# Optimization experiments

Measured on AMD Instinct MI355X. Metric: run time of the kernel, lower is better.

## Reference

```python
import jax, jax.numpy as jnp
import numpy as np

NUM_HEADS = 16
ROPE_BASE = 10000.0

def rotate_half(x):
    h = x.shape[-1] // 2
    return jnp.concatenate([-x[..., h:], x[..., :h]], axis=-1)

def rope_cos_sin(seq_len, head_dim, dtype):
    inv_freq = 1.0 / (ROPE_BASE ** (jnp.arange(0, head_dim, 2, dtype=jnp.float32) / head_dim))
    t = jnp.arange(seq_len, dtype=jnp.float32)
    freqs = jnp.outer(t, inv_freq)              # [N, hd/2]
    emb = jnp.concatenate([freqs, freqs], -1)   # [N, hd]
    return jnp.cos(emb).astype(dtype), jnp.sin(emb).astype(dtype)

def setup_inputs() -> dict:
    key = jax.random.key(0)
    ks = jax.random.split(key, 5)
    B, N, D = 2, 2048, 1024
    s = 1.0 / np.sqrt(D)
    return {
        "x": jax.random.normal(ks[0], (B, N, D), jnp.float32),
        "attention_mask": jnp.ones((B, N), jnp.int32),
        "Wq": jax.random.normal(ks[1], (D, D), jnp.float32) * s,
        "Wk": jax.random.normal(ks[2], (D, D), jnp.float32) * s,
        "Wv": jax.random.normal(ks[3], (D, D), jnp.float32) * s,
        "Wo": jax.random.normal(ks[4], (D, D), jnp.float32) * s,
    }

def reference(x, attention_mask, Wq, Wk, Wv, Wo):
    B, N, D = x.shape
    H = NUM_HEADS
    hd = D // H
    scale = hd ** -0.5
    # projections (nn.Linear: x @ W.T), split heads -> [B, H, N, hd]
    q = jnp.einsum('bnd,ed->bne', x, Wq).reshape(B, N, H, hd).transpose(0, 2, 1, 3)
    k = jnp.einsum('bnd,ed->bne', x, Wk).reshape(B, N, H, hd).transpose(0, 2, 1, 3)
    v = jnp.einsum('bnd,ed->bne', x, Wv).reshape(B, N, H, hd).transpose(0, 2, 1, 3)
    cos, sin = rope_cos_sin(N, hd, x.dtype)     # [N, hd]
    cos = cos[None, None]; sin = sin[None, None]
    q = q * cos + rotate_half(q) * sin
    k = k * cos + rotate_half(k) * sin
    attn = jnp.einsum('bhqd,bhkd->bhqk', q, k) * scale
    mask = attention_mask.astype(bool)[:, None, None, :]        # [B,1,1,N]
    attn = jnp.where(mask, attn, -jnp.inf)
    all_masked = (attention_mask.sum(-1) == 0)[:, None, None, None]
    attn = jnp.where(all_masked, 0.0, attn)
    attn = jax.nn.softmax(attn, axis=-1)
    out = jnp.einsum('bhqk,bhkd->bhqd', attn, v)
    out = out.transpose(0, 2, 1, 3).reshape(B, N, D)
    return jnp.einsum('bnd,ed->bne', out, Wo)
```

## Files before the change

### kernel.cpp

```cpp
#include <hip/hip_runtime.h>
#include <math.h>

#define BATCH 2
#define SEQ   2048
#define DM    1024
#define NH    16
#define HD    64
#define MTOT  (BATCH*SEQ)

typedef short v8s __attribute__((ext_vector_type(8)));
typedef short v4s __attribute__((ext_vector_type(4)));
typedef float v4f __attribute__((ext_vector_type(4)));

#define MFMA16(a, b, c) __builtin_amdgcn_mfma_f32_16x16x32_bf16((a), (b), (c), 0, 0, 0)

__device__ __forceinline__ short f2b(float f) {
    union { float f; unsigned u; } v; v.f = f;
    return (short)((v.u + 0x8000u) >> 16);
}

__global__ __launch_bounds__(256) void cvt_all_kernel(
    const float* __restrict__ x,  const float* __restrict__ wq,
    const float* __restrict__ wk, const float* __restrict__ wv,
    const float* __restrict__ wo, short* __restrict__ dst)
{
    int i = blockIdx.x * 256 + threadIdx.x;
    const float* src; int off;
    if (i < (1 << 19)) { src = x; off = i; }
    else {
        int j = i - (1 << 19);
        int wsel = j >> 17;
        off = j & ((1 << 17) - 1);
        src = (wsel == 0) ? wq : (wsel == 1) ? wk : (wsel == 2) ? wv : wo;
    }
    const float4* s4 = (const float4*)src;
    float4 a = s4[2 * off], b = s4[2 * off + 1];
    v8s p;
    p[0] = f2b(a.x); p[1] = f2b(a.y); p[2] = f2b(a.z); p[3] = f2b(a.w);
    p[4] = f2b(b.x); p[5] = f2b(b.y); p[6] = f2b(b.z); p[7] = f2b(b.w);
    *(v8s*)&dst[8 * i] = p;
}

__global__ __launch_bounds__(256, 2) void kv_rope_mfma(
    const short* __restrict__ xb, const short* __restrict__ Wkb,
    const short* __restrict__ Wvb, short* __restrict__ K, short* __restrict__ Vt)
{
    const int zz = blockIdx.z;
    const short* __restrict__ Wb = zz ? Wvb : Wkb;
    const int m0 = blockIdx.x * 128, e00 = blockIdx.y * 128;
    const int tid = threadIdx.x;
    const int w = tid >> 6, lane = tid & 63, lq = lane >> 4, lr = lane & 15;
    const int wm = w >> 1, wn = w & 1;

    __shared__ union {
        struct { short As[128][32]; short Bs[128][32]; } p1;
        short Css[128][136];
    } u;

    v4f acc[4][4];
    #pragma unroll
    for (int i = 0; i < 4; ++i)
        for (int j = 0; j < 4; ++j)
            for (int r = 0; r < 4; ++r) acc[i][j][r] = 0.f;

    const int arow = tid >> 1, aseg = (tid & 1) * 16;
    for (int k0 = 0; k0 < DM; k0 += 32) {
        v8s a0 = *(const v8s*)&xb[(size_t)(m0 + arow) * DM + k0 + aseg];
        v8s a1 = *(const v8s*)&xb[(size_t)(m0 + arow) * DM + k0 + aseg + 8];
        v8s b0 = *(const v8s*)&Wb[(size_t)(e00 + arow) * DM + k0 + aseg];
        v8s b1 = *(const v8s*)&Wb[(size_t)(e00 + arow) * DM + k0 + aseg + 8];
        __syncthreads();
        *(v8s*)&u.p1.As[arow][aseg] = a0;
        *(v8s*)&u.p1.As[arow][aseg + 8] = a1;
        *(v8s*)&u.p1.Bs[arow][aseg] = b0;
        *(v8s*)&u.p1.Bs[arow][aseg + 8] = b1;
        __syncthreads();
        v8s af[4], bf[4];
        #pragma unroll
        for (int i = 0; i < 4; ++i)
            af[i] = *(const v8s*)&u.p1.As[64 * wm + 16 * i + lr][8 * lq];
        #pragma unroll
        for (int j = 0; j < 4; ++j)
            bf[j] = *(const v8s*)&u.p1.Bs[64 * wn + 16 * j + lr][8 * lq];
        #pragma unroll
        for (int i = 0; i < 4; ++i)
            #pragma unroll
            for (int j = 0; j < 4; ++j)
                acc[i][j] = MFMA16(af[i], bf[j], acc[i][j]);
    }
    __syncthreads();

    const int b = m0 >> 11, n00 = m0 & (SEQ - 1);
    const float LN1E4_D32 = 0.28782313662425572f;

    if (zz == 0) {
        float f0 = expf(-(float)lr * LN1E4_D32);
        float f1 = expf(-(float)(16 + lr) * LN1E4_D32);
        #pragma unroll
        for (int i = 0; i < 4; ++i) {
            #pragma unroll
            for (int r = 0; r < 4; ++r) {
                int row = 64 * wm + 16 * i + 4 * lq + r;
                int n = n00 + row;
                float c0v, s0v, c1v, s1v;
                sincosf((float)n * f0, &s0v, &c0v);
                sincosf((float)n * f1, &s1v, &c1v);
                float q0 = acc[i][0][r], q1 = acc[i][1][r];
                float q2 = acc[i][2][r], q3 = acc[i][3][r];
                u.Css[row][64 * wn + lr]      = f2b(q0 * c0v - q2 * s0v);
                u.Css[row][64 * wn + 16 + lr] = f2b(q1 * c1v - q3 * s1v);
                u.Css[row][64 * wn + 32 + lr] = f2b(q2 * c0v + q0 * s0v);
                u.Css[row][64 * wn + 48 + lr] = f2b(q3 * c1v + q1 * s1v);
            }
        }
        __syncthreads();
        int row = tid >> 1, hh = tid & 1;
        int h = (e00 >> 6) + hh;
        int n = n00 + row;
        size_t base = (((size_t)(b * NH + h)) * SEQ + n) * HD;
        #pragma unroll
        for (int p = 0; p < 8; ++p)
            *(v8s*)&K[base + 8 * p] = *(const v8s*)&u.Css[row][64 * hh + 8 * p];
    } else {
        #pragma unroll
        for (int i = 0; i < 4; ++i) {
            #pragma unroll
            for (int j = 0; j < 4; ++j) {
                v4s t;
                #pragma unroll
                for (int r = 0; r < 4; ++r) t[r] = f2b(acc[i][j][r]);
                *(v4s*)&u.Css[64 * wn + 16 * j + lr][64 * wm + 16 * i + 4 * lq] = t;
            }
        }
        __syncthreads();
        int c = tid >> 1, half = (tid & 1) * 64;
        int h = (e00 + c) >> 6, d = (e00 + c) & 63;
        size_t base = (((size_t)(b * NH + h)) * HD + d) * SEQ + n00 + half;
        #pragma unroll
        for (int p = 0; p < 8; ++p)
            *(v8s*)&Vt[base + 8 * p] = *(const v8s*)&u.Css[c][half + 8 * p];
    }
}

__global__ __launch_bounds__(256, 2) void attn_mfma(
    const short* __restrict__ xb, const short* __restrict__ Wqb,
    const short* __restrict__ K, const short* __restrict__ Vt,
    const int* __restrict__ mask, short* __restrict__ O)
{
    const int m0 = blockIdx.x * 128, h = blockIdx.y, e0 = h * 64;
    const int b = m0 >> 11, n0 = m0 & (SEQ - 1), bh = b * NH + h;
    const int tid = threadIdx.x;
    const int w = tid >> 6, lane = tid & 63, lq = lane >> 4, lr = lane & 15;
    const int sr = tid >> 2, sc = (tid & 3) * 8;

    __shared__ union {
        struct { short As[128][32]; short Bs[64][32]; } p1;
        struct { short Ks[64][72]; short Vs[64][72]; } p2;
    } u;
    __shared__ short Ps[128][72];
    __shared__ float mbias[64];

    v4f acc[2][4];
    #pragma unroll
    for (int s = 0; s < 2; ++s)
        for (int nt = 0; nt < 4; ++nt)
            for (int r = 0; r < 4; ++r) acc[s][nt][r] = 0.f;

    for (int k0 = 0; k0 < DM; k0 += 32) {
        v8s a0 = *(const v8s*)&xb[(size_t)(m0 + sr) * DM + k0 + sc];
        v8s a1 = *(const v8s*)&xb[(size_t)(m0 + 64 + sr) * DM + k0 + sc];
        v8s bv = *(const v8s*)&Wqb[(size_t)(e0 + sr) * DM + k0 + sc];
        __syncthreads();
        *(v8s*)&u.p1.As[sr][sc] = a0;
        *(v8s*)&u.p1.As[64 + sr][sc] = a1;
        *(v8s*)&u.p1.Bs[sr][sc] = bv;
        __syncthreads();
        v8s aw0 = *(const v8s*)&u.p1.As[16 * w + lr][lq * 8];
        v8s aw1 = *(const v8s*)&u.p1.As[64 + 16 * w + lr][lq * 8];
        #pragma unroll
        for (int nt = 0; nt < 4; ++nt) {
            v8s bb = *(const v8s*)&u.p1.Bs[16 * nt + lr][lq * 8];
            acc[0][nt] = MFMA16(aw0, bb, acc[0][nt]);
            acc[1][nt] = MFMA16(aw1, bb, acc[1][nt]);
        }
    }

    {
        const float LN1E4_D32 = 0.28782313662425572f;
        const float QSCALE = 0.18033688011112042f;
        float f0 = expf(-(float)lr * LN1E4_D32);
        float f1 = expf(-(float)(16 + lr) * LN1E4_D32);
        #pragma unroll
        for (int s = 0; s < 2; ++s) {
            #pragma unroll
            for (int r = 0; r < 4; ++r) {
                int n = n0 + 64 * s + 16 * w + 4 * lq + r;
                float c0v, s0v, c1v, s1v;
                sincosf((float)n * f0, &s0v, &c0v);
                sincosf((float)n * f1, &s1v, &c1v);
                float q0 = acc[s][0][r], q1 = acc[s][1][r];
                float q2 = acc[s][2][r], q3 = acc[s][3][r];
                Ps[64 * s + 16 * w + 4 * lq + r][lr]      = f2b(QSCALE * (q0 * c0v - q2 * s0v));
                Ps[64 * s + 16 * w + 4 * lq + r][16 + lr] = f2b(QSCALE * (q1 * c1v - q3 * s1v));
                Ps[64 * s + 16 * w + 4 * lq + r][32 + lr] = f2b(QSCALE * (q2 * c0v + q0 * s0v));
                Ps[64 * s + 16 * w + 4 * lq + r][48 + lr] = f2b(QSCALE * (q3 * c1v + q1 * s1v));
            }
        }
    }
    v8s aq[2][2];
    #pragma unroll
    for (int s = 0; s < 2; ++s)
        #pragma unroll
        for (int ks = 0; ks < 2; ++ks)
            aq[s][ks] = *(const v8s*)&Ps[64 * s + 16 * w + lr][32 * ks + 8 * lq];

    float lacc[2][4];
    #pragma unroll
    for (int s = 0; s < 2; ++s)
        for (int r = 0; r < 4; ++r) lacc[s][r] = 0.f;
    v4f o[2][4];
    #pragma unroll
    for (int s = 0; s < 2; ++s)
        for (int nt = 0; nt < 4; ++nt)
            for (int r = 0; r < 4; ++r) o[s][nt][r] = 0.f;

    const int r2 = tid >> 2, cc = (tid & 3) * 16;
    const int pr = 16 * (r2 & 3) + (r2 >> 2);
    const short* __restrict__ Kb = K + (size_t)bh * SEQ * HD;
    const short* __restrict__ Vb = Vt + (size_t)bh * HD * SEQ;

    v8s k1 = *(const v8s*)&Kb[(size_t)r2 * HD + cc];
    v8s k2 = *(const v8s*)&Kb[(size_t)r2 * HD + cc + 8];
    v8s v1 = *(const v8s*)&Vb[(size_t)r2 * SEQ + cc];
    v8s v2 = *(const v8s*)&Vb[(size_t)r2 * SEQ + cc + 8];
    int mnext = (tid < 64) ? mask[b * SEQ + tid] : 0;

    for (int c0 = 0; c0 < SEQ; c0 += 64) {
        __syncthreads();
        *(v8s*)&u.p2.Ks[pr][cc] = k1;
        *(v8s*)&u.p2.Ks[pr][cc + 8] = k2;
        *(v8s*)&u.p2.Vs[r2][cc] = v1;
        *(v8s*)&u.p2.Vs[r2][cc + 8] = v2;
        if (tid < 64) mbias[tid] = mnext ? -24.0f : -1e30f;
        __syncthreads();
        if (c0 + 64 < SEQ) {
            k1 = *(const v8s*)&Kb[(size_t)(c0 + 64 + r2) * HD + cc];
            k2 = *(const v8s*)&Kb[(size_t)(c0 + 64 + r2) * HD + cc + 8];
            v1 = *(const v8s*)&Vb[(size_t)r2 * SEQ + c0 + 64 + cc];
            v2 = *(const v8s*)&Vb[(size_t)r2 * SEQ + c0 + 64 + cc + 8];
            if (tid < 64) mnext = mask[b * SEQ + c0 + 64 + tid];
        }

        v8s kf[2][4], vf[2][4];
        #pragma unroll
        for (int ks = 0; ks < 2; ++ks)
            #pragma unroll
            for (int nt = 0; nt < 4; ++nt) {
                kf[ks][nt] = *(const v8s*)&u.p2.Ks[16 * nt + lr][32 * ks + 8 * lq];
                vf[ks][nt] = *(const v8s*)&u.p2.Vs[16 * nt + lr][32 * ks + 8 * lq];
            }
        float bias[4];
        #pragma unroll
        for (int nt = 0; nt < 4; ++nt) bias[nt] = mbias[4 * lr + nt];

        #pragma unroll
        for (int s = 0; s < 2; ++s) {
            v4f sv[4];
            #pragma unroll
            for (int nt = 0; nt < 4; ++nt)
                for (int r = 0; r < 4; ++r) sv[nt][r] = 0.f;
            #pragma unroll
            for (int ks = 0; ks < 2; ++ks)
                #pragma unroll
                for (int nt = 0; nt < 4; ++nt)
                    sv[nt] = MFMA16(aq[s][ks], kf[ks][nt], sv[nt]);

            #pragma unroll
            for (int r = 0; r < 4; ++r) {
                v4s pk;
                #pragma unroll
                for (int nt = 0; nt < 4; ++nt) {
                    float p = exp2f(sv[nt][r] + bias[nt]);
                    lacc[s][r] += p;
                    pk[nt] = f2b(p);
                }
                *(v4s*)&Ps[64 * s + 16 * w + 4 * lq + r][4 * lr] = pk;
            }
            #pragma unroll
            for (int ks = 0; ks < 2; ++ks) {
                v8s a = *(const v8s*)&Ps[64 * s + 16 * w + lr][32 * ks + 8 * lq];
                #pragma unroll
                for (int nt = 0; nt < 4; ++nt)
                    o[s][nt] = MFMA16(a, vf[ks][nt], o[s][nt]);
            }
        }
    }

    #pragma unroll
    for (int s = 0; s < 2; ++s) {
        #pragma unroll
        for (int r = 0; r < 4; ++r) {
            float l = lacc[s][r];
            l += __shfl_xor(l, 1);
            l += __shfl_xor(l, 2);
            l += __shfl_xor(l, 4);
            l += __shfl_xor(l, 8);
            float inv = (l > 0.f) ? 1.f / l : 0.f;
            int qrow = 64 * s + 16 * w + 4 * lq + r;
            #pragma unroll
            for (int nt = 0; nt < 4; ++nt)
                O[(size_t)(m0 + qrow) * DM + h * HD + 16 * nt + lr] =
                    f2b(o[s][nt][r] * inv);
        }
    }
}

__global__ __launch_bounds__(256, 2) void oproj_mfma(
    const short* __restrict__ O, const short* __restrict__ Wob,
    float* __restrict__ out)
{
    const int m0 = blockIdx.x * 64, e00 = blockIdx.y * 128;
    const int tid = threadIdx.x;
    const int w = tid >> 6, lane = tid & 63, lq = lane >> 4, lr = lane & 15;

    __shared__ short As[64][32];
    __shared__ short Bs[128][32];

    v4f acc[4][2];
    #pragma unroll
    for (int i = 0; i < 4; ++i)
        for (int j = 0; j < 2; ++j)
            for (int r = 0; r < 4; ++r) acc[i][j][r] = 0.f;

    const int arow = tid >> 2, aseg = (tid & 3) * 8;
    const int brow = tid >> 1, bseg = (tid & 1) * 16;
    for (int k0 = 0; k0 < DM; k0 += 32) {
        v8s a0 = *(const v8s*)&O[(size_t)(m0 + arow) * DM + k0 + aseg];
        v8s b0 = *(const v8s*)&Wob[(size_t)(e00 + brow) * DM + k0 + bseg];
        v8s b1 = *(const v8s*)&Wob[(size_t)(e00 + brow) * DM + k0 + bseg + 8];
        __syncthreads();
        *(v8s*)&As[arow][aseg] = a0;
        *(v8s*)&Bs[brow][bseg] = b0;
        *(v8s*)&Bs[brow][bseg + 8] = b1;
        __syncthreads();
        v8s af[4], bf[2];
        #pragma unroll
        for (int i = 0; i < 4; ++i)
            af[i] = *(const v8s*)&As[16 * i + lr][8 * lq];
        #pragma unroll
        for (int j = 0; j < 2; ++j)
            bf[j] = *(const v8s*)&Bs[32 * w + 16 * j + lr][8 * lq];
        #pragma unroll
        for (int i = 0; i < 4; ++i)
            #pragma unroll
            for (int j = 0; j < 2; ++j)
                acc[i][j] = MFMA16(af[i], bf[j], acc[i][j]);
    }

    #pragma unroll
    for (int i = 0; i < 4; ++i)
        #pragma unroll
        for (int r = 0; r < 4; ++r) {
            int m = m0 + 16 * i + 4 * lq + r;
            #pragma unroll
            for (int j = 0; j < 2; ++j)
                out[(size_t)m * DM + e00 + 32 * w + 16 * j + lr] = acc[i][j][r];
        }
}

extern "C" void kernel_launch(void* const* d_in, const int* in_sizes, int n_in,
                              void* d_out, int out_size, void* d_ws, size_t ws_size,
                              hipStream_t stream)
{
    const float* x    = (const float*)d_in[0];
    const int*   mask = (const int*)d_in[1];
    const float* Wq   = (const float*)d_in[2];
    const float* Wk   = (const float*)d_in[3];
    const float* Wv   = (const float*)d_in[4];
    const float* Wo   = (const float*)d_in[5];
    float* out = (float*)d_out;

    short* xb  = (short*)d_ws;
    short* Wqb = xb  + (size_t)MTOT * DM;
    short* Wkb = Wqb + (size_t)DM * DM;
    short* Wvb = Wkb + (size_t)DM * DM;
    short* Wob = Wvb + (size_t)DM * DM;
    short* O   = Wob + (size_t)DM * DM;
    short* K  = (short*)d_out;
    short* Vt = K + (size_t)MTOT * DM;

    cvt_all_kernel<<<4096, 256, 0, stream>>>(x, Wq, Wk, Wv, Wo, xb);

    dim3 g1(MTOT / 128, DM / 128, 2);
    kv_rope_mfma<<<g1, 256, 0, stream>>>(xb, Wkb, Wvb, K, Vt);

    dim3 g2(MTOT / 128, NH);
    attn_mfma<<<g2, 256, 0, stream>>>(xb, Wqb, K, Vt, mask, O);

    dim3 g3(MTOT / 64, DM / 128);
    oproj_mfma<<<g3, 256, 0, stream>>>(O, Wob, out);
}
```

Measured before the change: 221.8 us.

## Split attention block across 8 waves and use fast range-reduced RoPE sincos

The attention kernel now launches 512 threads per 128-query block, so each wave owns 16 query rows instead of 32. This halves per-wave accumulator registers and spreads K/V tile loads across more threads, aiming for higher occupancy and latency hiding. RoPE sin/cos is computed by reducing the angle to revolutions with floor and calling __sinf/__cosf instead of full-precision sincosf, in both the KV and Q paths. The trade-offs are some loss of accuracy at large angles and the Wq tile being loaded by only half the threads.

```diff
diff --git a/kernel.cpp b/kernel.cpp
--- a/kernel.cpp
+++ b/kernel.cpp
@@ -18,6 +18,17 @@
     union { float f; unsigned u; } v; v.f = f;
     return (short)((v.u + 0x8000u) >> 16);
 }
+
+__device__ __forceinline__ void rope_cs(int n, float f_rev, float* c, float* s) {
+    float rev = (float)n * f_rev;
+    float t = rev - floorf(rev);
+    float ang = t * 6.283185307179586f;
+    *c = __cosf(ang);
+    *s = __sinf(ang);
+}
+
+#define L2_1E4_D32 0.4152410118609203f
+#define INV2PI     0.15915494309189535f
 
 __global__ __launch_bounds__(256) void cvt_all_kernel(
     const float* __restrict__ x,  const float* __restrict__ wq,
@@ -91,11 +102,10 @@
     __syncthreads();
 
     const int b = m0 >> 11, n00 = m0 & (SEQ - 1);
-    const float LN1E4_D32 = 0.28782313662425572f;
 
     if (zz == 0) {
-        float f0 = expf(-(float)lr * LN1E4_D32);
-        float f1 = expf(-(float)(16 + lr) * LN1E4_D32);
+        float f0 = exp2f(-(float)lr * L2_1E4_D32) * INV2PI;
+        float f1 = exp2f(-(float)(16 + lr) * L2_1E4_D32) * INV2PI;
         #pragma unroll
         for (int i = 0; i < 4; ++i) {
             #pragma unroll
@@ -103,8 +113,8 @@
                 int row = 64 * wm + 16 * i + 4 * lq + r;
                 int n = n00 + row;
                 float c0v, s0v, c1v, s1v;
-                sincosf((float)n * f0, &s0v, &c0v);
-                sincosf((float)n * f1, &s1v, &c1v);
+                rope_cs(n, f0, &c0v, &s0v);
+                rope_cs(n, f1, &c1v, &s1v);
                 float q0 = acc[i][0][r], q1 = acc[i][1][r];
                 float q2 = acc[i][2][r], q3 = acc[i][3][r];
                 u.Css[row][64 * wn + lr]      = f2b(q0 * c0v - q2 * s0v);
@@ -142,7 +152,7 @@
     }
 }
 
-__global__ __launch_bounds__(256, 2) void attn_mfma(
+__global__ __launch_bounds__(512, 4) void attn_mfma(
     const short* __restrict__ xb, const short* __restrict__ Wqb,
     const short* __restrict__ K, const short* __restrict__ Vt,
     const int* __restrict__ mask, short* __restrict__ O)
@@ -151,7 +161,6 @@
     const int b = m0 >> 11, n0 = m0 & (SEQ - 1), bh = b * NH + h;
     const int tid = threadIdx.x;
     const int w = tid >> 6, lane = tid & 63, lq = lane >> 4, lr = lane & 15;
-    const int sr = tid >> 2, sc = (tid & 3) * 8;
 
     __shared__ union {
         struct { short As[128][32]; short Bs[64][32]; } p1;
@@ -160,94 +169,79 @@
     __shared__ short Ps[128][72];
     __shared__ float mbias[64];
 
-    v4f acc[2][4];
-    #pragma unroll
-    for (int s = 0; s < 2; ++s)
-        for (int nt = 0; nt < 4; ++nt)
-            for (int r = 0; r < 4; ++r) acc[s][nt][r] = 0.f;
-
+    v4f acc[4];
+    #pragma unroll
+    for (int nt = 0; nt < 4; ++nt)
+        for (int r = 0; r < 4; ++r) acc[nt][r] = 0.f;
+
+    const int sr = tid >> 2, sc = (tid & 3) * 8;
+    const int br = (tid - 256) >> 2, bc = (tid & 3) * 8;
     for (int k0 = 0; k0 < DM; k0 += 32) {
         v8s a0 = *(const v8s*)&xb[(size_t)(m0 + sr) * DM + k0 + sc];
-        v8s a1 = *(const v8s*)&xb[(size_t)(m0 + 64 + sr) * DM + k0 + sc];
-        v8s bv = *(const v8s*)&Wqb[(size_t)(e0 + sr) * DM + k0 + sc];
+        v8s bv;
+        if (tid >= 256)
+            bv = *(const v8s*)&Wqb[(size_t)(e0 + br) * DM + k0 + bc];
         __syncthreads();
         *(v8s*)&u.p1.As[sr][sc] = a0;
-        *(v8s*)&u.p1.As[64 + sr][sc] = a1;
-        *(v8s*)&u.p1.Bs[sr][sc] = bv;
-        __syncthreads();
-        v8s aw0 = *(const v8s*)&u.p1.As[16 * w + lr][lq * 8];
-        v8s aw1 = *(const v8s*)&u.p1.As[64 + 16 * w + lr][lq * 8];
+        if (tid >= 256)
+            *(v8s*)&u.p1.Bs[br][bc] = bv;
+        __syncthreads();
+        v8s aw = *(const v8s*)&u.p1.As[16 * w + lr][8 * lq];
         #pragma unroll
         for (int nt = 0; nt < 4; ++nt) {
-            v8s bb = *(const v8s*)&u.p1.Bs[16 * nt + lr][lq * 8];
-            acc[0][nt] = MFMA16(aw0, bb, acc[0][nt]);
-            acc[1][nt] = MFMA16(aw1, bb, acc[1][nt]);
+            v8s bb = *(const v8s*)&u.p1.Bs[16 * nt + lr][8 * lq];
+            acc[nt] = MFMA16(aw, bb, acc[nt]);
         }
     }
 
     {
-        const float LN1E4_D32 = 0.28782313662425572f;
         const float QSCALE = 0.18033688011112042f;
-        float f0 = expf(-(float)lr * LN1E4_D32);
-        float f1 = expf(-(float)(16 + lr) * LN1E4_D32);
-        #pragma unroll
-        for (int s = 0; s < 2; ++s) {
-            #pragma unroll
-            for (int r = 0; r < 4; ++r) {
-                int n = n0 + 64 * s + 16 * w + 4 * lq + r;
-                float c0v, s0v, c1v, s1v;
-                sincosf((float)n * f0, &s0v, &c0v);
-                sincosf((float)n * f1, &s1v, &c1v);
-                float q0 = acc[s][0][r], q1 = acc[s][1][r];
-                float q2 = acc[s][2][r], q3 = acc[s][3][r];
-                Ps[64 * s + 16 * w + 4 * lq + r][lr]      = f2b(QSCALE * (q0 * c0v - q2 * s0v));
-                Ps[64 * s + 16 * w + 4 * lq + r][16 + lr] = f2b(QSCALE * (q1 * c1v - q3 * s1v));
-                Ps[64 * s + 16 * w + 4 * lq + r][32 + lr] = f2b(QSCALE * (q2 * c0v + q0 * s0v));
-                Ps[64 * s + 16 * w + 4 * lq + r][48 + lr] = f2b(QSCALE * (q3 * c1v + q1 * s1v));
-            }
-        }
-    }
-    v8s aq[2][2];
-    #pragma unroll
-    for (int s = 0; s < 2; ++s)
-        #pragma unroll
-        for (int ks = 0; ks < 2; ++ks)
-            aq[s][ks] = *(const v8s*)&Ps[64 * s + 16 * w + lr][32 * ks + 8 * lq];
-
-    float lacc[2][4];
-    #pragma unroll
-    for (int s = 0; s < 2; ++s)
-        for (int r = 0; r < 4; ++r) lacc[s][r] = 0.f;
-    v4f o[2][4];
-    #pragma unroll
-    for (int s = 0; s < 2; ++s)
-        for (int nt = 0; nt < 4; ++nt)
-            for (int r = 0; r < 4; ++r) o[s][nt][r] = 0.f;
-
-    const int r2 = tid >> 2, cc = (tid & 3) * 16;
-    const int pr = 16 * (r2 & 3) + (r2 >> 2);
+        float f0 = exp2f(-(float)lr * L2_1E4_D32) * INV2PI;
+        float f1 = exp2f(-(float)(16 + lr) * L2_1E4_D32) * INV2PI;
+        #pragma unroll
+        for (int r = 0; r < 4; ++r) {
+            int row = 16 * w + 4 * lq + r;
+            int n = n0 + row;
+            float c0v, s0v, c1v, s1v;
+            rope_cs(n, f0, &c0v, &s0v);
+            rope_cs(n, f1, &c1v, &s1v);
+            float q0 = acc[0][r], q1 = acc[1][r];
+            float q2 = acc[2][r], q3 = acc[3][r];
+            Ps[row][lr]      = f2b(QSCALE * (q0 * c0v - q2 * s0v));
+            Ps[row][16 + lr] = f2b(QSCALE * (q1 * c1v - q3 * s1v));
+            Ps[row][32 + lr] = f2b(QSCALE * (q2 * c0v + q0 * s0v));
+            Ps[row][48 + lr] = f2b(QSCALE * (q3 * c1v + q1 * s1v));
+        }
+    }
+    v8s aq[2];
+    #pragma unroll
+    for (int ks = 0; ks < 2; ++ks)
+        aq[ks] = *(const v8s*)&Ps[16 * w + lr][32 * ks + 8 * lq];
+
+    float lacc[4] = {0.f, 0.f, 0.f, 0.f};
+    v4f o[4];
+    #pragma unroll
+    for (int nt = 0; nt < 4; ++nt)
+        for (int r = 0; r < 4; ++r) o[nt][r] = 0.f;
+
+    const int kr = tid >> 3, kc = (tid & 7) * 8;
+    const int pr = 16 * (kr & 3) + (kr >> 2);
     const short* __restrict__ Kb = K + (size_t)bh * SEQ * HD;
     const short* __restrict__ Vb = Vt + (size_t)bh * HD * SEQ;
 
-    v8s k1 = *(const v8s*)&Kb[(size_t)r2 * HD + cc];
-    v8s k2 = *(const v8s*)&Kb[(size_t)r2 * HD + cc + 8];
-    v8s v1 = *(const v8s*)&Vb[(size_t)r2 * SEQ + cc];
-    v8s v2 = *(const v8s*)&Vb[(size_t)r2 * SEQ + cc + 8];
+    v8s k1 = *(const v8s*)&Kb[(size_t)kr * HD + kc];
+    v8s v1 = *(const v8s*)&Vb[(size_t)kr * SEQ + kc];
     int mnext = (tid < 64) ? mask[b * SEQ + tid] : 0;
 
     for (int c0 = 0; c0 < SEQ; c0 += 64) {
         __syncthreads();
-        *(v8s*)&u.p2.Ks[pr][cc] = k1;
-        *(v8s*)&u.p2.Ks[pr][cc + 8] = k2;
-        *(v8s*)&u.p2.Vs[r2][cc] = v1;
-        *(v8s*)&u.p2.Vs[r2][cc + 8] = v2;
+        *(v8s*)&u.p2.Ks[pr][kc] = k1;
+        *(v8s*)&u.p2.Vs[kr][kc] = v1;
         if (tid < 64) mbias[tid] = mnext ? -24.0f : -1e30f;
         __syncthreads();
         if (c0 + 64 < SEQ) {
-            k1 = *(const v8s*)&Kb[(size_t)(c0 + 64 + r2) * HD + cc];
-            k2 = *(const v8s*)&Kb[(size_t)(c0 + 64 + r2) * HD + cc + 8];
-            v1 = *(const v8s*)&Vb[(size_t)r2 * SEQ + c0 + 64 + cc];
-            v2 = *(const v8s*)&Vb[(size_t)r2 * SEQ + c0 + 64 + cc + 8];
+            k1 = *(const v8s*)&Kb[(size_t)(c0 + 64 + kr) * HD + kc];
+            v1 = *(const v8s*)&Vb[(size_t)kr * SEQ + c0 + 64 + kc];
             if (tid < 64) mnext = mask[b * SEQ + c0 + 64 + tid];
         }
 
@@ -263,55 +257,49 @@
         #pragma unroll
         for (int nt = 0; nt < 4; ++nt) bias[nt] = mbias[4 * lr + nt];
 
-        #pragma unroll
-        for (int s = 0; s < 2; ++s) {
-            v4f sv[4];
+        v4f sv[4];
+        #pragma unroll
+        for (int nt = 0; nt < 4; ++nt)
+            for (int r = 0; r < 4; ++r) sv[nt][r] = 0.f;
+        #pragma unroll
+        for (int ks = 0; ks < 2; ++ks)
             #pragma unroll
             for (int nt = 0; nt < 4; ++nt)
-                for (int r = 0; r < 4; ++r) sv[nt][r] = 0.f;
-            #pragma unroll
-            for (int ks = 0; ks < 2; ++ks)
-                #pragma unroll
-                for (int nt = 0; nt < 4; ++nt)
-                    sv[nt] = MFMA16(aq[s][ks], kf[ks][nt], sv[nt]);
-
-            #pragma unroll
-            for (int r = 0; r < 4; ++r) {
-                v4s pk;
-                #pragma unroll
-                for (int nt = 0; nt < 4; ++nt) {
-                    float p = exp2f(sv[nt][r] + bias[nt]);
-                    lacc[s][r] += p;
-                    pk[nt] = f2b(p);
-                }
-                *(v4s*)&Ps[64 * s + 16 * w + 4 * lq + r][4 * lr] = pk;
+                sv[nt] = MFMA16(aq[ks], kf[ks][nt], sv[nt]);
+
+        #pragma unroll
+        for (int r = 0; r < 4; ++r) {
+            v4s pk;
+            #pragma unroll
+            for (int nt = 0; nt < 4; ++nt) {
+                float p = exp2f(sv[nt][r] + bias[nt]);
+                lacc[r] += p;
+                pk[nt] = f2b(p);
             }
-            #pragma unroll
-            for (int ks = 0; ks < 2; ++ks) {
-                v8s a = *(const v8s*)&Ps[64 * s + 16 * w + lr][32 * ks + 8 * lq];
-                #pragma unroll
-                for (int nt = 0; nt < 4; ++nt)
-                    o[s][nt] = MFMA16(a, vf[ks][nt], o[s][nt]);
-            }
-        }
-    }
-
-    #pragma unroll
-    for (int s = 0; s < 2; ++s) {
-        #pragma unroll
-        for (int r = 0; r < 4; ++r) {
-            float l = lacc[s][r];
-            l += __shfl_xor(l, 1);
-            l += __shfl_xor(l, 2);
-            l += __shfl_xor(l, 4);
-            l += __shfl_xor(l, 8);
-            float inv = (l > 0.f) ? 1.f / l : 0.f;
-            int qrow = 64 * s + 16 * w + 4 * lq + r;
+            *(v4s*)&Ps[16 * w + 4 * lq + r][4 * lr] = pk;
+        }
+        #pragma unroll
+        for (int ks = 0; ks < 2; ++ks) {
+            v8s a = *(const v8s*)&Ps[16 * w + lr][32 * ks + 8 * lq];
             #pragma unroll
             for (int nt = 0; nt < 4; ++nt)
-                O[(size_t)(m0 + qrow) * DM + h * HD + 16 * nt + lr] =
-                    f2b(o[s][nt][r] * inv);
-        }
+                o[nt] = MFMA16(a, vf[ks][nt], o[nt]);
+        }
+    }
+
+    #pragma unroll
+    for (int r = 0; r < 4; ++r) {
+        float l = lacc[r];
+        l += __shfl_xor(l, 1);
+        l += __shfl_xor(l, 2);
+        l += __shfl_xor(l, 4);
+        l += __shfl_xor(l, 8);
+        float inv = (l > 0.f) ? 1.f / l : 0.f;
+        int qrow = 16 * w + 4 * lq + r;
+        #pragma unroll
+        for (int nt = 0; nt < 4; ++nt)
+            O[(size_t)(m0 + qrow) * DM + h * HD + 16 * nt + lr] =
+                f2b(o[nt][r] * inv);
     }
 }
 
@@ -395,7 +383,7 @@
     kv_rope_mfma<<<g1, 256, 0, stream>>>(xb, Wkb, Wvb, K, Vt);
 
     dim3 g2(MTOT / 128, NH);
-    attn_mfma<<<g2, 256, 0, stream>>>(xb, Wqb, K, Vt, mask, O);
+    attn_mfma<<<g2, 512, 0, stream>>>(xb, Wqb, K, Vt, mask, O);
 
     dim3 g3(MTOT / 64, DM / 128);
     oproj_mfma<<<g3, 256, 0, stream>>>(O, Wob, out);
```

Result: no change. 218.9 us (-1.3%).
